# Performance work log

Measured on AMD Instinct MI355X. Metric: run time of the kernel, lower is better.

## Reference

```python
import jax, jax.numpy as jnp
import numpy as np

N_ENTS = 50000
N_EDGES = 500000
N_RELS = 200
RANK = 128
N_LAYERS = 2
RRELU_SLOPE = (1.0 / 8.0 + 1.0 / 3.0) / 2.0  # F.rrelu eval-mode: mean of default lower/upper


def setup_inputs() -> dict:
    key = jax.random.key(0)
    ks = jax.random.split(key, 9)
    return {
        "ent_emb": jax.random.normal(ks[0], (N_ENTS, RANK), dtype=jnp.float32),
        "rel_emb": jax.random.normal(ks[1], (N_RELS, RANK), dtype=jnp.float32),
        "norm": jax.random.uniform(ks[2], (N_ENTS, 1), dtype=jnp.float32),
        "Wn": jax.random.normal(ks[3], (N_LAYERS, RANK, RANK), dtype=jnp.float32) * 0.05,
        "Wl": jax.random.normal(ks[4], (N_LAYERS, RANK, RANK), dtype=jnp.float32) * 0.05,
        "Wa": jax.random.normal(ks[5], (N_LAYERS, RANK, RANK), dtype=jnp.float32) * 0.05,
        "src": jax.random.randint(ks[6], (N_EDGES,), 0, N_ENTS, dtype=jnp.int32),
        "dst": jax.random.randint(ks[7], (N_EDGES,), 0, N_ENTS, dtype=jnp.int32),
        "etype": jax.random.randint(ks[8], (N_EDGES,), 0, N_RELS, dtype=jnp.int32),
    }


def reference(ent_emb, rel_emb, norm, Wn, Wl, Wa, src, dst, etype):
    n = ent_emb.shape[0]
    # in-degree mask (same graph across layers)
    in_deg = jax.ops.segment_sum(jnp.ones_like(dst, dtype=jnp.float32), dst, num_segments=n)
    has_in = (in_deg > 0)[:, None]  # [N,1]
    h = ent_emb
    for l in range(Wn.shape[0]):
        # edge gather + add + linear: msg = (h[src] + rel_emb[etype]) @ Wn[l]
        msg = (h[src] + rel_emb[etype]) @ Wn[l]  # [E, rank]
        # scatter-sum into destination nodes, then per-node norm
        agg = jax.ops.segment_sum(msg, dst, num_segments=n) * norm  # [N, rank]
        # masked self-loop: loop_weight where in_degree>0, else alone_loop_weight
        loop = jnp.where(has_in, h @ Wl[l], h @ Wa[l])
        h = agg + loop
        # rrelu in eval mode == leaky relu with slope (1/8 + 1/3)/2
        h = jnp.where(h >= 0, h, h * RRELU_SLOPE)
        # dropout=0.0 -> identity
    return h
```

## Files before the change

### kernel.cpp

```cpp
#include <hip/hip_runtime.h>

#define SLOPE 0.22916666666666666f
#define ALONE_CAP 2048

typedef __attribute__((ext_vector_type(8))) short bfrag;
typedef __attribute__((ext_vector_type(4))) float ffrag;

__device__ __forceinline__ unsigned short rne16(float f) {
    unsigned u = __float_as_uint(f);
    return (unsigned short)((u + 0x7FFFu + ((u >> 16) & 1u)) >> 16);
}
__device__ __forceinline__ float bf2f(unsigned short h) {
    return __uint_as_float(((unsigned)h) << 16);
}
__device__ __forceinline__ unsigned packsplit(float f) {
    unsigned short hi = rne16(f);
    unsigned short lo = rne16(f - bf2f(hi));
    return ((unsigned)hi << 16) | lo;
}
__device__ __forceinline__ float recon(unsigned u) {
    return __uint_as_float(u & 0xFFFF0000u) + __uint_as_float(u << 16);
}
__device__ __forceinline__ float4 recon4(uint4 u) {
    return make_float4(recon(u.x), recon(u.y), recon(u.z), recon(u.w));
}

__global__ __launch_bounds__(256) void prep_kernel(
    const int* __restrict__ dst, int* __restrict__ deg, int e, int eb,
    const float* __restrict__ ent, unsigned* __restrict__ Esp,
    int total4, int cb,
    const float* __restrict__ Wn, const float* __restrict__ Wl,
    ushort* __restrict__ packW) {
    int b = blockIdx.x;
    if (b < eb) {
        int i = b * 256 + threadIdx.x;
        if (i < e) atomicAdd(&deg[dst[i]], 1);
    } else if (b < eb + cb) {
        int i = (b - eb) * 256 + threadIdx.x;
        if (i >= total4) return;
        float4 v = ((const float4*)ent)[i];
        uint4 w;
        w.x = packsplit(v.x); w.y = packsplit(v.y);
        w.z = packsplit(v.z); w.w = packsplit(v.w);
        ((uint4*)Esp)[i] = w;
    } else {
        int t = (b - eb - cb) * 256 + threadIdx.x;
        if (t >= 4 * 4 * 128 * 4) return;
        int quad = t & 3;
        int nn   = (t >> 2) & 127;
        int kc   = (t >> 9) & 3;
        int mat  = t >> 11;
        const float* W = ((mat & 1) ? Wl : Wn) + (mat >> 1) * 16384;
        ushort* oh = packW + mat * 32768;
        ushort* ol = oh + 16384;
        int obase = ((kc * 128 + nn) * 4 + quad) * 8;
        #pragma unroll
        for (int j = 0; j < 8; ++j) {
            float w = W[(kc * 32 + quad * 8 + j) * 128 + nn];
            unsigned short hi = rne16(w);
            oh[obase + j] = hi;
            ol[obase + j] = rne16(w - bf2f(hi));
        }
    }
}

__global__ __launch_bounds__(256) void scan_partial_kernel(const int* __restrict__ deg,
                                                           int* __restrict__ partial, int n) {
    __shared__ int wsum[4];
    int base = blockIdx.x * 1024;
    int t = threadIdx.x;
    int s = 0;
    #pragma unroll
    for (int j = 0; j < 4; ++j) {
        int i = base + t + 256 * j;
        if (i < n) s += deg[i];
    }
    #pragma unroll
    for (int off = 1; off < 64; off <<= 1) s += __shfl_xor(s, off, 64);
    if ((t & 63) == 0) wsum[t >> 6] = s;
    __syncthreads();
    if (t == 0) partial[blockIdx.x] = wsum[0] + wsum[1] + wsum[2] + wsum[3];
}

__global__ __launch_bounds__(256) void scan_final_kernel(const int* __restrict__ deg,
                                                         const int* __restrict__ partial,
                                                         int* __restrict__ row_off,
                                                         int* __restrict__ alone_list,
                                                         int* __restrict__ alone_count, int n) {
    __shared__ int wsum[4];
    __shared__ int sbase;
    int bid = blockIdx.x;
    int t = threadIdx.x, lane = t & 63, wid = t >> 6;
    if (wid == 0) {
        int v = (lane < bid) ? partial[lane] : 0;
        #pragma unroll
        for (int off = 1; off < 64; off <<= 1) v += __shfl_xor(v, off, 64);
        if (lane == 0) sbase = v;
    }
    int base = bid * 1024;
    int i0 = base + t * 4;
    int v0 = (i0 + 0 < n) ? deg[i0 + 0] : 0;
    int v1 = (i0 + 1 < n) ? deg[i0 + 1] : 0;
    int v2 = (i0 + 2 < n) ? deg[i0 + 2] : 0;
    int v3 = (i0 + 3 < n) ? deg[i0 + 3] : 0;
    int s = v0 + v1 + v2 + v3;
    int x = s;
    #pragma unroll
    for (int off = 1; off < 64; off <<= 1) {
        int y = __shfl_up(x, off, 64);
        if (lane >= off) x += y;
    }
    if (lane == 63) wsum[wid] = x;
    __syncthreads();
    int wbase = 0;
    #pragma unroll
    for (int w = 0; w < 4; ++w) { int ws = wsum[w]; if (w < wid) wbase += ws; }
    int p = sbase + wbase + x - s;
    if (i0 + 0 <= n) row_off[i0 + 0] = p;
    p += v0;
    if (i0 + 1 <= n) row_off[i0 + 1] = p;
    p += v1;
    if (i0 + 2 <= n) row_off[i0 + 2] = p;
    p += v2;
    if (i0 + 3 <= n) row_off[i0 + 3] = p;
    if (i0 + 0 < n && v0 == 0) { int q = atomicAdd(alone_count, 1); if (q < ALONE_CAP) alone_list[q] = i0; }
    if (i0 + 1 < n && v1 == 0) { int q = atomicAdd(alone_count, 1); if (q < ALONE_CAP) alone_list[q] = i0 + 1; }
    if (i0 + 2 < n && v2 == 0) { int q = atomicAdd(alone_count, 1); if (q < ALONE_CAP) alone_list[q] = i0 + 2; }
    if (i0 + 3 < n && v3 == 0) { int q = atomicAdd(alone_count, 1); if (q < ALONE_CAP) alone_list[q] = i0 + 3; }
}

__global__ __launch_bounds__(256) void scatter_kernel(
    const int* __restrict__ src, const int* __restrict__ dst,
    const int* __restrict__ ety, const int* __restrict__ row_off,
    int* __restrict__ cursor, unsigned* __restrict__ edges, int e) {
    int i = blockIdx.x * 256 + threadIdx.x;
    if (i < e) {
        int v = dst[i];
        int pos = row_off[v] + atomicAdd(&cursor[v], 1);
        edges[pos] = (unsigned)src[i] | ((unsigned)ety[i] << 16);
    }
}

template <int SPLIT>
__global__ __launch_bounds__(256) void agg_kernel(
    const float* __restrict__ hf, const unsigned* __restrict__ hs,
    const float* __restrict__ rel,
    const float* __restrict__ norm, const int* __restrict__ row_off,
    const unsigned* __restrict__ edges, unsigned* __restrict__ Ssp, int n) {
    int wave = threadIdx.x >> 6, lane = threadIdx.x & 63;
    int v = blockIdx.x * 4 + wave;
    if (v >= n) return;
    int s0 = row_off[v], s1 = row_off[v + 1];
    float nm = norm[v];
    int half = lane >> 5;
    int c4 = (lane & 31) * 4;
    float4 acc = make_float4(0.f, 0.f, 0.f, 0.f);
    int e = s0;
    for (; e + 7 < s1; e += 8) {
        unsigned q0 = edges[e + half];
        unsigned q1 = edges[e + 2 + half];
        unsigned q2 = edges[e + 4 + half];
        unsigned q3 = edges[e + 6 + half];
        float4 h0, h1, h2, h3;
        if (SPLIT) {
            h0 = recon4(*(const uint4*)&hs[(size_t)(q0 & 0xFFFFu) * 128 + c4]);
            h1 = recon4(*(const uint4*)&hs[(size_t)(q1 & 0xFFFFu) * 128 + c4]);
            h2 = recon4(*(const uint4*)&hs[(size_t)(q2 & 0xFFFFu) * 128 + c4]);
            h3 = recon4(*(const uint4*)&hs[(size_t)(q3 & 0xFFFFu) * 128 + c4]);
        } else {
            h0 = *(const float4*)&hf[(size_t)(q0 & 0xFFFFu) * 128 + c4];
            h1 = *(const float4*)&hf[(size_t)(q1 & 0xFFFFu) * 128 + c4];
            h2 = *(const float4*)&hf[(size_t)(q2 & 0xFFFFu) * 128 + c4];
            h3 = *(const float4*)&hf[(size_t)(q3 & 0xFFFFu) * 128 + c4];
        }
        float4 r0 = *(const float4*)&rel[(size_t)(q0 >> 16) * 128 + c4];
        float4 r1 = *(const float4*)&rel[(size_t)(q1 >> 16) * 128 + c4];
        float4 r2 = *(const float4*)&rel[(size_t)(q2 >> 16) * 128 + c4];
        float4 r3 = *(const float4*)&rel[(size_t)(q3 >> 16) * 128 + c4];
        acc.x += ((h0.x + r0.x) + (h1.x + r1.x)) + ((h2.x + r2.x) + (h3.x + r3.x));
        acc.y += ((h0.y + r0.y) + (h1.y + r1.y)) + ((h2.y + r2.y) + (h3.y + r3.y));
        acc.z += ((h0.z + r0.z) + (h1.z + r1.z)) + ((h2.z + r2.z) + (h3.z + r3.z));
        acc.w += ((h0.w + r0.w) + (h1.w + r1.w)) + ((h2.w + r2.w) + (h3.w + r3.w));
    }
    for (; e + 1 < s1; e += 2) {
        unsigned q0 = edges[e + half];
        float4 h0 = SPLIT ? recon4(*(const uint4*)&hs[(size_t)(q0 & 0xFFFFu) * 128 + c4])
                          : *(const float4*)&hf[(size_t)(q0 & 0xFFFFu) * 128 + c4];
        float4 r0 = *(const float4*)&rel[(size_t)(q0 >> 16) * 128 + c4];
        acc.x += h0.x + r0.x; acc.y += h0.y + r0.y;
        acc.z += h0.z + r0.z; acc.w += h0.w + r0.w;
    }
    if (e < s1 && half == 0) {
        unsigned q0 = edges[e];
        float4 h0 = SPLIT ? recon4(*(const uint4*)&hs[(size_t)(q0 & 0xFFFFu) * 128 + c4])
                          : *(const float4*)&hf[(size_t)(q0 & 0xFFFFu) * 128 + c4];
        float4 r0 = *(const float4*)&rel[(size_t)(q0 >> 16) * 128 + c4];
        acc.x += h0.x + r0.x; acc.y += h0.y + r0.y;
        acc.z += h0.z + r0.z; acc.w += h0.w + r0.w;
    }
    acc.x += __shfl_xor(acc.x, 32, 64);
    acc.y += __shfl_xor(acc.y, 32, 64);
    acc.z += __shfl_xor(acc.z, 32, 64);
    acc.w += __shfl_xor(acc.w, 32, 64);
    if (half == 0) {
        uint4 w;
        w.x = packsplit(acc.x * nm); w.y = packsplit(acc.y * nm);
        w.z = packsplit(acc.z * nm); w.w = packsplit(acc.w * nm);
        *(uint4*)&Ssp[(size_t)v * 128 + c4] = w;
    }
}

__global__ __launch_bounds__(128) void gemm_mfma_kernel(
    const unsigned* __restrict__ Ssp, const unsigned* Hsp,
    const ushort* __restrict__ Pnh, const ushort* __restrict__ Pnl,
    const ushort* __restrict__ Plh, const ushort* __restrict__ Pll,
    float* __restrict__ out, unsigned* Osp, int n) {
    const int tid = threadIdx.x;
    const int wave = tid >> 6, lane = tid & 63;
    const int quad = lane >> 4, l16 = lane & 15;
    const int row_base = blockIdx.x * 64 + wave * 32;

    int r0c = row_base + l16;       if (r0c > n - 1) r0c = n - 1;
    int r1c = row_base + 16 + l16;  if (r1c > n - 1) r1c = n - 1;

    ffrag acc[2][8];
    #pragma unroll
    for (int rt = 0; rt < 2; ++rt)
        #pragma unroll
        for (int ct = 0; ct < 8; ++ct) acc[rt][ct] = (ffrag)0.f;

    #pragma unroll 1
    for (int half = 0; half < 2; ++half) {
        const unsigned* A = half ? Hsp : Ssp;
        const ushort* Pbh = half ? Plh : Pnh;
        const ushort* Pbl = half ? Pll : Pnl;
        #pragma unroll 1
        for (int kc = 0; kc < 4; ++kc) {
            const int koff = kc * 32 + quad * 8;
            uint4 a0a = *(const uint4*)(A + (size_t)r0c * 128 + koff);
            uint4 a0b = *(const uint4*)(A + (size_t)r0c * 128 + koff + 4);
            uint4 a1a = *(const uint4*)(A + (size_t)r1c * 128 + koff);
            uint4 a1b = *(const uint4*)(A + (size_t)r1c * 128 + koff + 4);
            bfrag ah[2], al[2];
            #pragma unroll
            for (int j = 0; j < 4; ++j) {
                unsigned u0 = ((const unsigned*)&a0a)[j];
                unsigned u1 = ((const unsigned*)&a0b)[j];
                ah[0][j]     = (short)(u0 >> 16); al[0][j]     = (short)(u0 & 0xFFFFu);
                ah[0][j + 4] = (short)(u1 >> 16); al[0][j + 4] = (short)(u1 & 0xFFFFu);
                unsigned u2 = ((const unsigned*)&a1a)[j];
                unsigned u3 = ((const unsigned*)&a1b)[j];
                ah[1][j]     = (short)(u2 >> 16); al[1][j]     = (short)(u2 & 0xFFFFu);
                ah[1][j + 4] = (short)(u3 >> 16); al[1][j + 4] = (short)(u3 & 0xFFFFu);
            }
            bfrag bh[8], bl[8];
            #pragma unroll
            for (int ct = 0; ct < 8; ++ct) {
                int bidx = ((kc * 128 + ct * 16 + l16) * 4 + quad) * 8;
                bh[ct] = *(const bfrag*)(Pbh + bidx);
                bl[ct] = *(const bfrag*)(Pbl + bidx);
            }
            #pragma unroll
            for (int rt = 0; rt < 2; ++rt)
                #pragma unroll
                for (int ct = 0; ct < 8; ++ct)
                    acc[rt][ct] = __builtin_amdgcn_mfma_f32_16x16x32_bf16(
                        ah[rt], bh[ct], acc[rt][ct], 0, 0, 0);
            #pragma unroll
            for (int rt = 0; rt < 2; ++rt)
                #pragma unroll
                for (int ct = 0; ct < 8; ++ct)
                    acc[rt][ct] = __builtin_amdgcn_mfma_f32_16x16x32_bf16(
                        ah[rt], bl[ct], acc[rt][ct], 0, 0, 0);
            #pragma unroll
            for (int rt = 0; rt < 2; ++rt)
                #pragma unroll
                for (int ct = 0; ct < 8; ++ct)
                    acc[rt][ct] = __builtin_amdgcn_mfma_f32_16x16x32_bf16(
                        al[rt], bh[ct], acc[rt][ct], 0, 0, 0);
        }
    }

    __syncthreads();

    #pragma unroll
    for (int rt = 0; rt < 2; ++rt) {
        #pragma unroll
        for (int ct = 0; ct < 8; ++ct) {
            #pragma unroll
            for (int rg = 0; rg < 4; ++rg) {
                int r = row_base + rt * 16 + quad * 4 + rg;
                if (r < n) {
                    int c = ct * 16 + l16;
                    float v = acc[rt][ct][rg];
                    v = v >= 0.f ? v : v * SLOPE;
                    if (out) out[(size_t)r * 128 + c] = v;
                    if (Osp) Osp[(size_t)r * 128 + c] = packsplit(v);
                }
            }
        }
    }
}

__global__ __launch_bounds__(128) void fixup_kernel(
    const float* __restrict__ Hrows, int by_node,
    const float* __restrict__ Wa,
    const int* __restrict__ alone_list, const int* __restrict__ alone_count,
    float* out, unsigned* Osp, float* asave) {
    int cnt = *alone_count;
    if (cnt > ALONE_CAP) cnt = ALONE_CAP;
    int t = threadIdx.x;
    for (int i = blockIdx.x; i < cnt; i += gridDim.x) {
        int v = alone_list[i];
        const float* hrow = Hrows + (size_t)(by_node ? v : i) * 128;
        float acc = 0.f;
        for (int k = 0; k < 128; ++k)
            acc += hrow[k] * Wa[k * 128 + t];
        float o = acc >= 0.f ? acc : acc * SLOPE;
        if (out) out[(size_t)v * 128 + t] = o;
        if (Osp) Osp[(size_t)v * 128 + t] = packsplit(o);
        if (asave) asave[(size_t)i * 128 + t] = o;
    }
}

extern "C" void kernel_launch(void* const* d_in, const int* in_sizes, int n_in,
                              void* d_out, int out_size, void* d_ws, size_t ws_size,
                              hipStream_t stream) {
    const float* ent  = (const float*)d_in[0];
    const float* rel  = (const float*)d_in[1];
    const float* norm = (const float*)d_in[2];
    const float* Wn   = (const float*)d_in[3];
    const float* Wl   = (const float*)d_in[4];
    const float* Wa   = (const float*)d_in[5];
    const int*   src  = (const int*)d_in[6];
    const int*   dst  = (const int*)d_in[7];
    const int*   ety  = (const int*)d_in[8];
    float* out = (float*)d_out;

    const int n = in_sizes[2];
    const int e = in_sizes[7];

    char* ws = (char*)d_ws;
    int* deg         = (int*)ws;
    int* cursor      = deg + n;
    int* alone_count = cursor + n;
    size_t zbytes = (size_t)(2 * n + 1) * sizeof(int);
    size_t p = (zbytes + 255) & ~(size_t)255;
    int* row_off = (int*)(ws + p);
    p += (((size_t)(n + 1) * 4) + 255) & ~(size_t)255;
    int* partial = (int*)(ws + p);
    p += 256;
    int* alone_list = (int*)(ws + p);
    p += (((size_t)ALONE_CAP * 4) + 255) & ~(size_t)255;
    float* asave = (float*)(ws + p);
    p += (((size_t)ALONE_CAP * 128 * 4) + 255) & ~(size_t)255;
    unsigned* edges = (unsigned*)(ws + p);
    p += (((size_t)e * 4) + 255) & ~(size_t)255;
    unsigned* Ssp = (unsigned*)(ws + p);
    p += (((size_t)n * 128 * 4) + 255) & ~(size_t)255;
    unsigned* Esp = (unsigned*)(ws + p);
    p += (((size_t)n * 128 * 4) + 255) & ~(size_t)255;
    ushort* packW = (ushort*)(ws + p);
    p += 4 * 32768 * 2;

    const int eb = (e + 255) / 256;
    const int cb = (n * 32 + 255) / 256;
    const int nparts = (n + 1023) / 1024;
    const int gb = (n + 63) / 64;
    const int ab = (n + 3) / 4;

    hipMemsetAsync(ws, 0, zbytes, stream);
    prep_kernel<<<eb + cb + 32, 256, 0, stream>>>(dst, deg, e, eb,
                                                  ent, Esp, n * 32, cb,
                                                  Wn, Wl, packW);
    scan_partial_kernel<<<nparts, 256, 0, stream>>>(deg, partial, n);
    scan_final_kernel<<<nparts, 256, 0, stream>>>(deg, partial, row_off,
                                                  alone_list, alone_count, n);
    scatter_kernel<<<eb, 256, 0, stream>>>(src, dst, ety, row_off, cursor, edges, e);

    agg_kernel<0><<<ab, 256, 0, stream>>>(ent, nullptr, rel, norm, row_off, edges, Ssp, n);
    gemm_mfma_kernel<<<gb, 128, 0, stream>>>(Ssp, Esp,
                                             packW, packW + 16384,
                                             packW + 32768, packW + 49152,
                                             nullptr, Esp, n);
    fixup_kernel<<<16, 128, 0, stream>>>(ent, 1, Wa, alone_list, alone_count,
                                         nullptr, Esp, asave);

    agg_kernel<1><<<ab, 256, 0, stream>>>(nullptr, Esp, rel, norm, row_off, edges, Ssp, n);
    gemm_mfma_kernel<<<gb, 128, 0, stream>>>(Ssp, Esp,
                                             packW + 65536, packW + 81920,
                                             packW + 98304, packW + 114688,
                                             out, nullptr, n);
    fixup_kernel<<<16, 128, 0, stream>>>(asave, 0, Wa + 16384, alone_list, alone_count,
                                         out, nullptr, nullptr);
}
```

Baseline: 296.2 us.

## Use 4 waves of 16 rows per GEMM block and prefetch A fragments

The MFMA GEMM kernel now runs 256 threads per block, each wave owning 16 rows instead of 32. This halves the accumulator register footprint and adds a launch-bounds occupancy hint. The two nested K loops are flattened into one 8-step loop that software-prefetches the next A fragment while the current MFMAs run, and the unneeded __syncthreads is removed. The trade-off is that each wave reuses every B fragment load across half as many rows, so weight-load traffic per row doubles.

New measurement: 316.5 us. 6.8% more time.

```diff
diff --git a/kernel.cpp b/kernel.cpp
--- a/kernel.cpp
+++ b/kernel.cpp
@@ -210,7 +210,7 @@
     }
 }
 
-__global__ __launch_bounds__(128) void gemm_mfma_kernel(
+__global__ __launch_bounds__(256, 3) void gemm_mfma_kernel(
     const unsigned* __restrict__ Ssp, const unsigned* Hsp,
     const ushort* __restrict__ Pnh, const ushort* __restrict__ Pnl,
     const ushort* __restrict__ Plh, const ushort* __restrict__ Pll,
@@ -218,85 +218,75 @@
     const int tid = threadIdx.x;
     const int wave = tid >> 6, lane = tid & 63;
     const int quad = lane >> 4, l16 = lane & 15;
-    const int row_base = blockIdx.x * 64 + wave * 32;
-
-    int r0c = row_base + l16;       if (r0c > n - 1) r0c = n - 1;
-    int r1c = row_base + 16 + l16;  if (r1c > n - 1) r1c = n - 1;
-
-    ffrag acc[2][8];
-    #pragma unroll
-    for (int rt = 0; rt < 2; ++rt)
-        #pragma unroll
-        for (int ct = 0; ct < 8; ++ct) acc[rt][ct] = (ffrag)0.f;
+    const int row_base = blockIdx.x * 64 + wave * 16;
+
+    int r0c = row_base + l16;
+    if (r0c > n - 1) r0c = n - 1;
+    const size_t arow = (size_t)r0c * 128;
+
+    ffrag acc[8];
+    #pragma unroll
+    for (int ct = 0; ct < 8; ++ct) acc[ct] = (ffrag)0.f;
+
+    uint4 a_cur0 = *(const uint4*)(Ssp + arow + quad * 8);
+    uint4 a_cur1 = *(const uint4*)(Ssp + arow + quad * 8 + 4);
 
     #pragma unroll 1
-    for (int half = 0; half < 2; ++half) {
-        const unsigned* A = half ? Hsp : Ssp;
-        const ushort* Pbh = half ? Plh : Pnh;
-        const ushort* Pbl = half ? Pll : Pnl;
-        #pragma unroll 1
-        for (int kc = 0; kc < 4; ++kc) {
-            const int koff = kc * 32 + quad * 8;
-            uint4 a0a = *(const uint4*)(A + (size_t)r0c * 128 + koff);
-            uint4 a0b = *(const uint4*)(A + (size_t)r0c * 128 + koff + 4);
-            uint4 a1a = *(const uint4*)(A + (size_t)r1c * 128 + koff);
-            uint4 a1b = *(const uint4*)(A + (size_t)r1c * 128 + koff + 4);
-            bfrag ah[2], al[2];
-            #pragma unroll
-            for (int j = 0; j < 4; ++j) {
-                unsigned u0 = ((const unsigned*)&a0a)[j];
-                unsigned u1 = ((const unsigned*)&a0b)[j];
-                ah[0][j]     = (short)(u0 >> 16); al[0][j]     = (short)(u0 & 0xFFFFu);
-                ah[0][j + 4] = (short)(u1 >> 16); al[0][j + 4] = (short)(u1 & 0xFFFFu);
-                unsigned u2 = ((const unsigned*)&a1a)[j];
-                unsigned u3 = ((const unsigned*)&a1b)[j];
-                ah[1][j]     = (short)(u2 >> 16); al[1][j]     = (short)(u2 & 0xFFFFu);
-                ah[1][j + 4] = (short)(u3 >> 16); al[1][j + 4] = (short)(u3 & 0xFFFFu);
-            }
-            bfrag bh[8], bl[8];
-            #pragma unroll
-            for (int ct = 0; ct < 8; ++ct) {
-                int bidx = ((kc * 128 + ct * 16 + l16) * 4 + quad) * 8;
-                bh[ct] = *(const bfrag*)(Pbh + bidx);
-                bl[ct] = *(const bfrag*)(Pbl + bidx);
-            }
-            #pragma unroll
-            for (int rt = 0; rt < 2; ++rt)
-                #pragma unroll
-                for (int ct = 0; ct < 8; ++ct)
-                    acc[rt][ct] = __builtin_amdgcn_mfma_f32_16x16x32_bf16(
-                        ah[rt], bh[ct], acc[rt][ct], 0, 0, 0);
-            #pragma unroll
-            for (int rt = 0; rt < 2; ++rt)
-                #pragma unroll
-                for (int ct = 0; ct < 8; ++ct)
-                    acc[rt][ct] = __builtin_amdgcn_mfma_f32_16x16x32_bf16(
-                        ah[rt], bl[ct], acc[rt][ct], 0, 0, 0);
-            #pragma unroll
-            for (int rt = 0; rt < 2; ++rt)
-                #pragma unroll
-                for (int ct = 0; ct < 8; ++ct)
-                    acc[rt][ct] = __builtin_amdgcn_mfma_f32_16x16x32_bf16(
-                        al[rt], bh[ct], acc[rt][ct], 0, 0, 0);
-        }
-    }
-
-    __syncthreads();
-
-    #pragma unroll
-    for (int rt = 0; rt < 2; ++rt) {
+    for (int it = 0; it < 8; ++it) {
+        const int kc = it & 3;
+        const ushort* Pbh = (it >= 4) ? Plh : Pnh;
+        const ushort* Pbl = (it >= 4) ? Pll : Pnl;
+
+        uint4 a_nxt0, a_nxt1;
+        if (it < 7) {
+            const unsigned* An = (it + 1 >= 4) ? Hsp : Ssp;
+            const int koffn = ((it + 1) & 3) * 32 + quad * 8;
+            a_nxt0 = *(const uint4*)(An + arow + koffn);
+            a_nxt1 = *(const uint4*)(An + arow + koffn + 4);
+        }
+
+        bfrag bh[8], bl[8];
         #pragma unroll
         for (int ct = 0; ct < 8; ++ct) {
-            #pragma unroll
-            for (int rg = 0; rg < 4; ++rg) {
-                int r = row_base + rt * 16 + quad * 4 + rg;
-                if (r < n) {
-                    int c = ct * 16 + l16;
-                    float v = acc[rt][ct][rg];
-                    v = v >= 0.f ? v : v * SLOPE;
-                    if (out) out[(size_t)r * 128 + c] = v;
-                    if (Osp) Osp[(size_t)r * 128 + c] = packsplit(v);
-                }
+            int bidx = ((kc * 128 + ct * 16 + l16) * 4 + quad) * 8;
+            bh[ct] = *(const bfrag*)(Pbh + bidx);
+            bl[ct] = *(const bfrag*)(Pbl + bidx);
+        }
+
+        bfrag ah, al;
+        #pragma unroll
+        for (int j = 0; j < 4; ++j) {
+            unsigned u0 = ((const unsigned*)&a_cur0)[j];
+            unsigned u1 = ((const unsigned*)&a_cur1)[j];
+            ah[j]     = (short)(u0 >> 16); al[j]     = (short)(u0 & 0xFFFFu);
+            ah[j + 4] = (short)(u1 >> 16); al[j + 4] = (short)(u1 & 0xFFFFu);
+        }
+
+        #pragma unroll
+        for (int ct = 0; ct < 8; ++ct)
+            acc[ct] = __builtin_amdgcn_mfma_f32_16x16x32_bf16(ah, bh[ct], acc[ct], 0, 0, 0);
+        #pragma unroll
+        for (int ct = 0; ct < 8; ++ct)
+            acc[ct] = __builtin_amdgcn_mfma_f32_16x16x32_bf16(ah, bl[ct], acc[ct], 0, 0, 0);
+        #pragma unroll
+        for (int ct = 0; ct < 8; ++ct)
+            acc[ct] = __builtin_amdgcn_mfma_f32_16x16x32_bf16(al, bh[ct], acc[ct], 0, 0, 0);
+
+        a_cur0 = a_nxt0;
+        a_cur1 = a_nxt1;
+    }
+
+    #pragma unroll
+    for (int ct = 0; ct < 8; ++ct) {
+        #pragma unroll
+        for (int rg = 0; rg < 4; ++rg) {
+            int r = row_base + quad * 4 + rg;
+            if (r < n) {
+                int c = ct * 16 + l16;
+                float v = acc[ct][rg];
+                v = v >= 0.f ? v : v * SLOPE;
+                if (out) out[(size_t)r * 128 + c] = v;
+                if (Osp) Osp[(size_t)r * 128 + c] = packsplit(v);
             }
         }
     }
@@ -379,7 +369,7 @@
     scatter_kernel<<<eb, 256, 0, stream>>>(src, dst, ety, row_off, cursor, edges, e);
 
     agg_kernel<0><<<ab, 256, 0, stream>>>(ent, nullptr, rel, norm, row_off, edges, Ssp, n);
-    gemm_mfma_kernel<<<gb, 128, 0, stream>>>(Ssp, Esp,
+    gemm_mfma_kernel<<<gb, 256, 0, stream>>>(Ssp, Esp,
                                              packW, packW + 16384,
                                              packW + 32768, packW + 49152,
                                              nullptr, Esp, n);
@@ -387,7 +377,7 @@
                                          nullptr, Esp, asave);
 
     agg_kernel<1><<<ab, 256, 0, stream>>>(nullptr, Esp, rel, norm, row_off, edges, Ssp, n);
-    gemm_mfma_kernel<<<gb, 128, 0, stream>>>(Ssp, Esp,
+    gemm_mfma_kernel<<<gb, 256, 0, stream>>>(Ssp, Esp,
                                              packW + 65536, packW + 81920,
                                              packW + 98304, packW + 114688,
                                              out, nullptr, n);
```
